# Optimization experiments

Measured on AMD Instinct MI355X. Metric: run time of the kernel, lower is better.

The kernel has to match this reference:

```python
import jax, jax.numpy as jnp
import numpy as np
import math

NUM_HEADS = 8

def setup_inputs() -> dict:
    key = jax.random.key(0)
    ks = jax.random.split(key, 5)
    b, h, w, c = 4, 128, 128, 256
    x = jax.random.normal(ks[0], (b, h, w, c), dtype=jnp.float32)
    scale = 1.0 / math.sqrt(c)  # keep weights reasonably scaled (kaiming-like)
    Wq = jax.random.normal(ks[1], (c, c), dtype=jnp.float32) * scale
    Wk = jax.random.normal(ks[2], (c, c), dtype=jnp.float32) * scale
    Wv = jax.random.normal(ks[3], (c, c), dtype=jnp.float32) * scale
    Wout = jax.random.normal(ks[4], (c, c), dtype=jnp.float32) * scale
    return {"x": x, "Wq": Wq, "Wk": Wk, "Wv": Wv, "Wout": Wout}

def reference(x, Wq, Wk, Wv, Wout):
    b, h, w, c = x.shape
    hw = h * w
    heads = NUM_HEADS
    dh = c // heads
    xs = x.reshape(b, hw, c)
    q = xs @ Wq  # (b, hw, c)
    k = xs @ Wk
    v = xs @ Wv

    def split_heads(t):
        # (b, hw, c) -> (b, c, hw) -> (b, heads, dh, hw)
        return t.transpose(0, 2, 1).reshape(b, heads, dh, hw)

    q = split_heads(q)
    k = split_heads(k)
    v = split_heads(v)
    # L2-normalize along the feature (hw) axis; original has no epsilon
    q = q / jnp.linalg.norm(q, axis=-1, keepdims=True)
    k = k / jnp.linalg.norm(k, axis=-1, keepdims=True)
    d_k = q.shape[-1]  # = hw
    attn = jnp.einsum('bhcd,bhed->bhce', q, k) / math.sqrt(d_k)  # (b,heads,dh,dh)
    attn = jax.nn.softmax(attn, axis=-1)
    vals = jnp.einsum('bhce,bhed->bhcd', attn, v)  # (b,heads,dh,hw)
    vals = vals.transpose(0, 3, 1, 2).reshape(b, hw, c)
    out = (vals @ Wout).reshape(b, h, w, c)
    return out
```

## Files before the change

### kernel.cpp

```cpp
#include <hip/hip_runtime.h>


#define B_   4
#define HW_  16384
#define C_   256

typedef __attribute__((ext_vector_type(8))) short short8;
typedef __attribute__((ext_vector_type(4))) float floatx4;

__device__ __forceinline__ unsigned short f2bf(float f) {
  unsigned u = __builtin_bit_cast(unsigned, f);
  u += 0x7FFFu + ((u >> 16) & 1u);
  return (unsigned short)(u >> 16);
}

__device__ __forceinline__ void gl_lds16(const unsigned short* g, unsigned short* l) {
  __builtin_amdgcn_global_load_lds(
      (const __attribute__((address_space(1))) unsigned int*)g,
      (__attribute__((address_space(3))) unsigned int*)l, 16, 0, 0);
}

__global__ __launch_bounds__(256) void k_cast_tr(const float* __restrict__ x,
                                                 unsigned short* __restrict__ xb,
                                                 unsigned short* __restrict__ xT) {
  __shared__ unsigned short lds[64][72];
  int bid = blockIdx.x;
  int t = threadIdx.x;
  int ct = bid & 3;
  int pt = (bid >> 2) & 255;
  int b  = bid >> 10;
  const float* src = x + ((size_t)(b * HW_ + pt * 64)) * C_ + ct * 64;
#pragma unroll
  for (int e = 0; e < 4; e++) {
    int lin = t + e * 256;
    int p = lin >> 4, c4 = lin & 15;
    float4 v = *(const float4*)(src + (size_t)p * C_ + c4 * 4);
    ushort4 h;
    h.x = f2bf(v.x); h.y = f2bf(v.y); h.z = f2bf(v.z); h.w = f2bf(v.w);
    *(ushort4*)(xb + ((size_t)(b * HW_ + pt * 64 + p)) * C_ + ct * 64 + c4 * 4) = h;
    lds[c4 * 4 + 0][p] = h.x;
    lds[c4 * 4 + 1][p] = h.y;
    lds[c4 * 4 + 2][p] = h.z;
    lds[c4 * 4 + 3][p] = h.w;
  }
  __syncthreads();
#pragma unroll
  for (int e = 0; e < 4; e++) {
    int lin = t + e * 256;
    int c = lin >> 4, p4 = lin & 15;
    ushort4 h;
    h.x = lds[c][p4 * 4 + 0];
    h.y = lds[c][p4 * 4 + 1];
    h.z = lds[c][p4 * 4 + 2];
    h.w = lds[c][p4 * 4 + 3];
    *(ushort4*)(xT + ((size_t)(b * C_ + ct * 64 + c)) * HW_ + pt * 64 + p4 * 4) = h;
  }
}

__global__ __launch_bounds__(256) void k_sgemm(const unsigned short* __restrict__ xT,
                                               float* __restrict__ part) {
  __shared__ unsigned short At[128 * 256];
  __shared__ unsigned short Bt[128 * 256];
  int bid = blockIdx.x;
  int ks = bid & 31, nt = (bid >> 5) & 1, mt = (bid >> 6) & 1, b = bid >> 7;
  const unsigned short* Ab = xT + ((size_t)(b * C_ + mt * 128)) * HW_ + ks * 512;
  const unsigned short* Bb = xT + ((size_t)(b * C_ + nt * 128)) * HW_ + ks * 512;
  int t = threadIdx.x, lane = t & 63, w = t >> 6;
  int wm = w >> 1, wn = w & 1;
  int l15 = lane & 15, l4 = lane >> 4;
  int lrow = lane >> 5;
  int lslot = lane & 31;
  floatx4 acc[4][4];
  floatx4 z = {0.f, 0.f, 0.f, 0.f};
#pragma unroll
  for (int i = 0; i < 4; i++)
#pragma unroll
    for (int j = 0; j < 4; j++) acc[i][j] = z;

  for (int ph = 0; ph < 2; ph++) {
    if (ph) __syncthreads();
#pragma unroll
    for (int i = 0; i < 16; i++) {
      int issue = w * 16 + i;
      int row = issue * 2 + lrow;
      int goct = lslot ^ (row & 31);
      gl_lds16(Ab + (size_t)row * HW_ + ph * 256 + goct * 8, At + issue * 512);
      gl_lds16(Bb + (size_t)row * HW_ + ph * 256 + goct * 8, Bt + issue * 512);
    }
    __syncthreads();
#pragma unroll
    for (int kk = 0; kk < 8; kk++) {
      short8 af[4], bfv[4];
      int oct = kk * 4 + l4;
#pragma unroll
      for (int tm = 0; tm < 4; tm++) {
        int row = wm * 64 + tm * 16 + l15;
        af[tm] = *(const short8*)(At + row * 256 + ((oct ^ (row & 31)) * 8));
      }
#pragma unroll
      for (int tn = 0; tn < 4; tn++) {
        int row = wn * 64 + tn * 16 + l15;
        bfv[tn] = *(const short8*)(Bt + row * 256 + ((oct ^ (row & 31)) * 8));
      }
#pragma unroll
      for (int tm = 0; tm < 4; tm++)
#pragma unroll
        for (int tn = 0; tn < 4; tn++)
          acc[tm][tn] = __builtin_amdgcn_mfma_f32_16x16x32_bf16(af[tm], bfv[tn],
                                                                acc[tm][tn], 0, 0, 0);
    }
  }
  float* pb = part + (size_t)bid * 16384;
#pragma unroll
  for (int tm = 0; tm < 4; tm++)
#pragma unroll
    for (int tn = 0; tn < 4; tn++)
#pragma unroll
      for (int r = 0; r < 4; r++) {
        int m = wm * 64 + tm * 16 + l4 * 4 + r;
        int n = wn * 64 + tn * 16 + l15;
        pb[m * 128 + n] = acc[tm][tn][r];
      }
}

__global__ __launch_bounds__(256) void k_sred(const float* __restrict__ part,
                                              float* __restrict__ S) {
  int idx = blockIdx.x * 256 + threadIdx.x;
  int b = idx >> 16;
  int m = (idx >> 8) & 255, n = idx & 255;
  const float* p = part + ((size_t)((b * 4 + (m >> 7) * 2 + (n >> 7)) * 32)) * 16384
                   + (m & 127) * 128 + (n & 127);
  float s = 0.f;
#pragma unroll
  for (int k = 0; k < 32; k++) s += p[k * 16384];
  S[idx] = s;
}

__global__ __launch_bounds__(256) void k_gemm_sw(const float* __restrict__ S,
                                                 const float* __restrict__ Wq,
                                                 const float* __restrict__ Wk,
                                                 float* __restrict__ SWq,
                                                 float* __restrict__ SWk) {
  __shared__ float As[64][17];
  __shared__ float Bs[16][65];
  int bid = blockIdx.x;
  int nt = bid & 7, mt = (bid >> 3) & 3, b = bid >> 5;
  int mb = mt * 64;
  const float* Wsel = (nt < 4) ? Wq : Wk;
  int nb = (nt & 3) * 64;
  int t = threadIdx.x, tx = t & 15, ty = t >> 4;
  float acc[4][4] = {};
  for (int kt = 0; kt < 16; kt++) {
    {
      int row = t >> 2, kq = t & 3;
      float4 v = *(const float4*)(S + ((size_t)(b * C_ + mb + row)) * C_ + kt * 16 + kq * 4);
      As[row][kq * 4 + 0] = v.x; As[row][kq * 4 + 1] = v.y;
      As[row][kq * 4 + 2] = v.z; As[row][kq * 4 + 3] = v.w;
    }
    {
      int kk = t >> 4, n4 = t & 15;
      float4 v = *(const float4*)(Wsel + ((size_t)(kt * 16 + kk)) * C_ + nb + n4 * 4);
      Bs[kk][n4 * 4 + 0] = v.x; Bs[kk][n4 * 4 + 1] = v.y;
      Bs[kk][n4 * 4 + 2] = v.z; Bs[kk][n4 * 4 + 3] = v.w;
    }
    __syncthreads();
#pragma unroll
    for (int k = 0; k < 16; k++) {
      float a[4], bb[4];
#pragma unroll
      for (int i = 0; i < 4; i++) a[i] = As[ty * 4 + i][k];
#pragma unroll
      for (int j = 0; j < 4; j++) bb[j] = Bs[k][tx * 4 + j];
#pragma unroll
      for (int i = 0; i < 4; i++)
#pragma unroll
        for (int j = 0; j < 4; j++) acc[i][j] += a[i] * bb[j];
    }
    __syncthreads();
  }
#pragma unroll
  for (int i = 0; i < 4; i++)
#pragma unroll
    for (int j = 0; j < 4; j++) {
      int row = mb + ty * 4 + i;
      int ng = nt * 64 + tx * 4 + j;
      if (ng < 256) SWq[((size_t)(b * C_ + row)) * C_ + ng] = acc[i][j];
      else          SWk[((size_t)(b * C_ + row)) * C_ + ng - 256] = acc[i][j];
    }
}

__global__ __launch_bounds__(256) void k_fuse(const float* __restrict__ Wq,
                                              const float* __restrict__ Wk,
                                              const float* __restrict__ SWq,
                                              const float* __restrict__ SWk,
                                              const float* __restrict__ Wout,
                                              float* __restrict__ U) {
  __shared__ float Wqh[256][32];
  __shared__ float Wkh[256][32];
  __shared__ float SWqh[256][32];
  __shared__ float SWkh[256][32];
  __shared__ float Lg[32][33];
  __shared__ float qp[8][32], kp[8][32], qin[32], kin[32];
  int b = blockIdx.x >> 3, h = blockIdx.x & 7;
  int t = threadIdx.x;
  int col = t & 31, rgrp = t >> 5;
  for (int r0 = 0; r0 < 256; r0 += 8) {
    int row = r0 + rgrp;
    Wqh[row][col]  = Wq[(size_t)row * C_ + h * 32 + col];
    Wkh[row][col]  = Wk[(size_t)row * C_ + h * 32 + col];
    SWqh[row][col] = SWq[((size_t)(b * C_ + row)) * C_ + h * 32 + col];
    SWkh[row][col] = SWk[((size_t)(b * C_ + row)) * C_ + h * 32 + col];
  }
  __syncthreads();
  {
    float g[4] = {0.f, 0.f, 0.f, 0.f};
    for (int k = 0; k < 256; k++) {
      float swk = SWkh[k][col];
#pragma unroll
      for (int r = 0; r < 4; r++) g[r] += Wqh[k][rgrp + 8 * r] * swk;
    }
#pragma unroll
    for (int r = 0; r < 4; r++) Lg[rgrp + 8 * r][col] = g[r];
  }
  {
    float sq = 0.f, sk = 0.f;
    for (int k = rgrp * 32; k < rgrp * 32 + 32; k++) {
      sq += Wqh[k][col] * SWqh[k][col];
      sk += Wkh[k][col] * SWkh[k][col];
    }
    qp[rgrp][col] = sq;
    kp[rgrp][col] = sk;
  }
  __syncthreads();
  if (t < 32) {
    float a = 0.f;
#pragma unroll
    for (int p = 0; p < 8; p++) a += qp[p][t];
    qin[t] = rsqrtf(a);
  } else if (t < 64) {
    int j = t - 32;
    float a = 0.f;
#pragma unroll
    for (int p = 0; p < 8; p++) a += kp[p][j];
    kin[j] = rsqrtf(a);
  }
  __syncthreads();
  if (t < 32) {
    float row[32];
    float mx = -1e30f;
#pragma unroll
    for (int j = 0; j < 32; j++) {
      row[j] = Lg[t][j] * qin[t] * kin[j] * 0.0078125f;
      mx = fmaxf(mx, row[j]);
    }
    float sum = 0.f;
#pragma unroll
    for (int j = 0; j < 32; j++) { row[j] = __expf(row[j] - mx); sum += row[j]; }
    float inv = 1.0f / sum;
#pragma unroll
    for (int j = 0; j < 32; j++) Lg[t][j] = row[j] * inv;
  }
  __syncthreads();
  float (*Wo)[256] = reinterpret_cast<float(*)[256]>(&Wqh[0][0]);
#pragma unroll
  for (int r = 0; r < 32; r++) Wo[r][t] = Wout[((size_t)(h * 32 + r)) * C_ + t];
  __syncthreads();
  for (int j = 0; j < 32; j++) {
    float a = 0.f;
#pragma unroll
    for (int i2 = 0; i2 < 32; i2++) a += Lg[i2][j] * Wo[i2][t];
    U[((size_t)(b * C_ + h * 32 + j)) * C_ + t] = a;
  }
}

__global__ __launch_bounds__(256) void k_gemm_w3(const float* __restrict__ Wv,
                                                 const float* __restrict__ U,
                                                 unsigned short* __restrict__ W3bT) {
  __shared__ float As[64][17];
  __shared__ float Bs[16][65];
  int bid = blockIdx.x;
  int nt = bid & 3, mt = (bid >> 2) & 3, b = bid >> 4;
  int mb = mt * 64, nb = nt * 64;
  int t = threadIdx.x, tx = t & 15, ty = t >> 4;
  float acc[4][4] = {};
  for (int kt = 0; kt < 16; kt++) {
    {
      int row = t >> 2, kq = t & 3;
      float4 v = *(const float4*)(Wv + ((size_t)(mb + row)) * C_ + kt * 16 + kq * 4);
      As[row][kq * 4 + 0] = v.x; As[row][kq * 4 + 1] = v.y;
      As[row][kq * 4 + 2] = v.z; As[row][kq * 4 + 3] = v.w;
    }
    {
      int kk = t >> 4, n4 = t & 15;
      float4 v = *(const float4*)(U + ((size_t)(b * C_ + kt * 16 + kk)) * C_ + nb + n4 * 4);
      Bs[kk][n4 * 4 + 0] = v.x; Bs[kk][n4 * 4 + 1] = v.y;
      Bs[kk][n4 * 4 + 2] = v.z; Bs[kk][n4 * 4 + 3] = v.w;
    }
    __syncthreads();
#pragma unroll
    for (int k = 0; k < 16; k++) {
      float a[4], bb[4];
#pragma unroll
      for (int i = 0; i < 4; i++) a[i] = As[ty * 4 + i][k];
#pragma unroll
      for (int j = 0; j < 4; j++) bb[j] = Bs[k][tx * 4 + j];
#pragma unroll
      for (int i = 0; i < 4; i++)
#pragma unroll
        for (int j = 0; j < 4; j++) acc[i][j] += a[i] * bb[j];
    }
    __syncthreads();
  }
#pragma unroll
  for (int i = 0; i < 4; i++)
#pragma unroll
    for (int j = 0; j < 4; j++)
      W3bT[((size_t)(b * C_ + nb + tx * 4 + j)) * C_ + mb + ty * 4 + i] = f2bf(acc[i][j]);
}

__global__ __launch_bounds__(256) void k_out(const unsigned short* __restrict__ xb,
                                             const unsigned short* __restrict__ W3bT,
                                             float* __restrict__ out) {
  __shared__ unsigned short At[128 * 64];
  __shared__ unsigned short Bt[128 * 64];
  int bid = blockIdx.x;
  int ntile = bid & 1, mtile = bid >> 1;
  int b = mtile >> 7;
  const unsigned short* Ab = xb + (size_t)mtile * 128 * C_;
  const unsigned short* Bb = W3bT + ((size_t)(b * C_ + ntile * 128)) * C_;
  int t = threadIdx.x, lane = t & 63, w = t >> 6;
  int wm = w >> 1, wn = w & 1;
  int l8 = lane >> 3, l7 = lane & 7;
  int srcoct = l7 ^ l8;
  int l15 = lane & 15, l4 = lane >> 4;
  floatx4 acc[4][4];
  floatx4 z = {0.f, 0.f, 0.f, 0.f};
#pragma unroll
  for (int i = 0; i < 4; i++)
#pragma unroll
    for (int j = 0; j < 4; j++) acc[i][j] = z;
  for (int s = 0; s < 4; s++) {
    if (s) __syncthreads();
#pragma unroll
    for (int i = 0; i < 4; i++) {
      int gi = w * 4 + i;
      int row = gi * 8 + l8;
      gl_lds16(Ab + (size_t)row * C_ + s * 64 + srcoct * 8, At + gi * 512);
      gl_lds16(Bb + (size_t)row * C_ + s * 64 + srcoct * 8, Bt + gi * 512);
    }
    __syncthreads();
#pragma unroll
    for (int kk = 0; kk < 2; kk++) {
      short8 af[4], bfv[4];
#pragma unroll
      for (int tm = 0; tm < 4; tm++) {
        int row = wm * 64 + tm * 16 + l15;
        int oct = kk * 4 + l4;
        af[tm] = *(const short8*)(At + row * 64 + ((oct ^ (l15 & 7)) * 8));
      }
#pragma unroll
      for (int tn = 0; tn < 4; tn++) {
        int row = wn * 64 + tn * 16 + l15;
        int oct = kk * 4 + l4;
        bfv[tn] = *(const short8*)(Bt + row * 64 + ((oct ^ (l15 & 7)) * 8));
      }
#pragma unroll
      for (int tm = 0; tm < 4; tm++)
#pragma unroll
        for (int tn = 0; tn < 4; tn++)
          acc[tm][tn] = __builtin_amdgcn_mfma_f32_16x16x32_bf16(af[tm], bfv[tn],
                                                                acc[tm][tn], 0, 0, 0);
    }
  }
  float* ob = out + (size_t)mtile * 128 * C_ + ntile * 128;
#pragma unroll
  for (int tm = 0; tm < 4; tm++)
#pragma unroll
    for (int tn = 0; tn < 4; tn++)
#pragma unroll
      for (int r = 0; r < 4; r++) {
        int m = wm * 64 + tm * 16 + l4 * 4 + r;
        int n = wn * 64 + tn * 16 + l15;
        ob[(size_t)m * C_ + n] = acc[tm][tn][r];
      }
}

extern "C" void kernel_launch(void* const* d_in, const int* in_sizes, int n_in,
                              void* d_out, int out_size, void* d_ws, size_t ws_size,
                              hipStream_t stream) {
  const float* x    = (const float*)d_in[0];
  const float* Wq   = (const float*)d_in[1];
  const float* Wk   = (const float*)d_in[2];
  const float* Wv   = (const float*)d_in[3];
  const float* Wout = (const float*)d_in[4];
  float* out = (float*)d_out;

  unsigned short* xT = (unsigned short*)d_ws;
  unsigned short* xb = xT + (size_t)16777216;
  float* part = (float*)(xb + (size_t)16777216);
  float* S    = part + (size_t)8388608;
  float* SWq  = S + 262144;
  float* SWk  = SWq + 262144;
  float* U    = SWk + 262144;
  unsigned short* W3bT = (unsigned short*)(U + 262144);

  k_cast_tr<<<dim3(4096), dim3(256), 0, stream>>>(x, xb, xT);
  k_sgemm<<<dim3(512), dim3(256), 0, stream>>>(xT, part);
  k_sred<<<dim3(1024), dim3(256), 0, stream>>>(part, S);
  k_gemm_sw<<<dim3(128), dim3(256), 0, stream>>>(S, Wq, Wk, SWq, SWk);
  k_fuse<<<dim3(32), dim3(256), 0, stream>>>(Wq, Wk, SWq, SWk, Wout, U);
  k_gemm_w3<<<dim3(64), dim3(256), 0, stream>>>(Wv, U, W3bT);
  k_out<<<dim3(1024), dim3(256), 0, stream>>>(xb, W3bT, out);
}
```

Baseline: 232.3 us.

## Drop bf16 x copy, fuse split-K reduction into SW gemm, halve splits

The cast kernel now writes only the transposed bf16 copy. The output GEMM reads fp32 x and fp32 W3T directly and converts to bf16 while staging into padded LDS, replacing the async global-to-LDS loads. The Gram GEMM uses 16 K-splits instead of 32, which halves the partial buffer. The separate reduction kernel is folded into the S·W GEMM, which also gets larger tiles. This removes one 32MB write and one kernel launch, but k_out now reads twice as many bytes of x, issues register-staged loads, and the fused SW kernel repeats the reduction for each block.

```diff
diff --git a/kernel.cpp b/kernel.cpp
--- a/kernel.cpp
+++ b/kernel.cpp
@@ -20,9 +20,8 @@
       (__attribute__((address_space(3))) unsigned int*)l, 16, 0, 0);
 }
 
-__global__ __launch_bounds__(256) void k_cast_tr(const float* __restrict__ x,
-                                                 unsigned short* __restrict__ xb,
-                                                 unsigned short* __restrict__ xT) {
+__global__ __launch_bounds__(256) void k_cast_t(const float* __restrict__ x,
+                                                unsigned short* __restrict__ xT) {
   __shared__ unsigned short lds[64][72];
   int bid = blockIdx.x;
   int t = threadIdx.x;
@@ -35,13 +34,10 @@
     int lin = t + e * 256;
     int p = lin >> 4, c4 = lin & 15;
     float4 v = *(const float4*)(src + (size_t)p * C_ + c4 * 4);
-    ushort4 h;
-    h.x = f2bf(v.x); h.y = f2bf(v.y); h.z = f2bf(v.z); h.w = f2bf(v.w);
-    *(ushort4*)(xb + ((size_t)(b * HW_ + pt * 64 + p)) * C_ + ct * 64 + c4 * 4) = h;
-    lds[c4 * 4 + 0][p] = h.x;
-    lds[c4 * 4 + 1][p] = h.y;
-    lds[c4 * 4 + 2][p] = h.z;
-    lds[c4 * 4 + 3][p] = h.w;
+    lds[c4 * 4 + 0][p] = f2bf(v.x);
+    lds[c4 * 4 + 1][p] = f2bf(v.y);
+    lds[c4 * 4 + 2][p] = f2bf(v.z);
+    lds[c4 * 4 + 3][p] = f2bf(v.w);
   }
   __syncthreads();
 #pragma unroll
@@ -62,9 +58,9 @@
   __shared__ unsigned short At[128 * 256];
   __shared__ unsigned short Bt[128 * 256];
   int bid = blockIdx.x;
-  int ks = bid & 31, nt = (bid >> 5) & 1, mt = (bid >> 6) & 1, b = bid >> 7;
-  const unsigned short* Ab = xT + ((size_t)(b * C_ + mt * 128)) * HW_ + ks * 512;
-  const unsigned short* Bb = xT + ((size_t)(b * C_ + nt * 128)) * HW_ + ks * 512;
+  int ks = bid & 15, nt = (bid >> 4) & 1, mt = (bid >> 5) & 1, b = bid >> 6;
+  const unsigned short* Ab = xT + ((size_t)(b * C_ + mt * 128)) * HW_ + ks * 1024;
+  const unsigned short* Bb = xT + ((size_t)(b * C_ + nt * 128)) * HW_ + ks * 1024;
   int t = threadIdx.x, lane = t & 63, w = t >> 6;
   int wm = w >> 1, wn = w & 1;
   int l15 = lane & 15, l4 = lane >> 4;
@@ -77,7 +73,7 @@
 #pragma unroll
     for (int j = 0; j < 4; j++) acc[i][j] = z;
 
-  for (int ph = 0; ph < 2; ph++) {
+  for (int ph = 0; ph < 4; ph++) {
     if (ph) __syncthreads();
 #pragma unroll
     for (int i = 0; i < 16; i++) {
@@ -123,70 +119,64 @@
       }
 }
 
-__global__ __launch_bounds__(256) void k_sred(const float* __restrict__ part,
-                                              float* __restrict__ S) {
-  int idx = blockIdx.x * 256 + threadIdx.x;
-  int b = idx >> 16;
-  int m = (idx >> 8) & 255, n = idx & 255;
-  const float* p = part + ((size_t)((b * 4 + (m >> 7) * 2 + (n >> 7)) * 32)) * 16384
-                   + (m & 127) * 128 + (n & 127);
-  float s = 0.f;
-#pragma unroll
-  for (int k = 0; k < 32; k++) s += p[k * 16384];
-  S[idx] = s;
-}
-
-__global__ __launch_bounds__(256) void k_gemm_sw(const float* __restrict__ S,
-                                                 const float* __restrict__ Wq,
-                                                 const float* __restrict__ Wk,
-                                                 float* __restrict__ SWq,
-                                                 float* __restrict__ SWk) {
-  __shared__ float As[64][17];
-  __shared__ float Bs[16][65];
+__global__ __launch_bounds__(256) void k_sw(const float* __restrict__ part,
+                                            const float* __restrict__ Wq,
+                                            const float* __restrict__ Wk,
+                                            float* __restrict__ SWq,
+                                            float* __restrict__ SWk) {
+  __shared__ float SsT[256][36];
+  __shared__ float Ws[128][132];
   int bid = blockIdx.x;
-  int nt = bid & 7, mt = (bid >> 3) & 3, b = bid >> 5;
-  int mb = mt * 64;
-  const float* Wsel = (nt < 4) ? Wq : Wk;
-  int nb = (nt & 3) * 64;
-  int t = threadIdx.x, tx = t & 15, ty = t >> 4;
+  int ns = bid & 3, ms = (bid >> 2) & 7, b = bid >> 5;
+  const float* Wsel = (ns < 2) ? Wq : Wk;
+  float* SWsel = (ns < 2) ? SWq : SWk;
+  int n0 = (ns & 1) * 128;
+  int t = threadIdx.x;
+  int nt_lane = t >> 7;
+  int cl = t & 127;
+#pragma unroll 4
+  for (int e = 0; e < 32; e++) {
+    int R = ms * 32 + e;
+    int mt = R >> 7;
+    const float* p = part + ((size_t)(((b * 2 + mt) * 2 + nt_lane) * 16)) * 16384
+                     + (R & 127) * 128 + cl;
+    float s = 0.f;
+#pragma unroll
+    for (int k = 0; k < 16; k++) s += p[(size_t)k * 16384];
+    SsT[t][e] = s;
+  }
+  int tx = t & 31, ty = t >> 5;
   float acc[4][4] = {};
-  for (int kt = 0; kt < 16; kt++) {
-    {
-      int row = t >> 2, kq = t & 3;
-      float4 v = *(const float4*)(S + ((size_t)(b * C_ + mb + row)) * C_ + kt * 16 + kq * 4);
-      As[row][kq * 4 + 0] = v.x; As[row][kq * 4 + 1] = v.y;
-      As[row][kq * 4 + 2] = v.z; As[row][kq * 4 + 3] = v.w;
-    }
-    {
-      int kk = t >> 4, n4 = t & 15;
-      float4 v = *(const float4*)(Wsel + ((size_t)(kt * 16 + kk)) * C_ + nb + n4 * 4);
-      Bs[kk][n4 * 4 + 0] = v.x; Bs[kk][n4 * 4 + 1] = v.y;
-      Bs[kk][n4 * 4 + 2] = v.z; Bs[kk][n4 * 4 + 3] = v.w;
+  for (int strip = 0; strip < 2; strip++) {
+    if (strip) __syncthreads();
+#pragma unroll
+    for (int e = 0; e < 16; e++) {
+      int idx = e * 256 + t;
+      int ml = idx >> 5, n4 = idx & 31;
+      float4 v = *(const float4*)(Wsel + ((size_t)(strip * 128 + ml)) * C_ + n0 + n4 * 4);
+      Ws[ml][n4 * 4 + 0] = v.x; Ws[ml][n4 * 4 + 1] = v.y;
+      Ws[ml][n4 * 4 + 2] = v.z; Ws[ml][n4 * 4 + 3] = v.w;
     }
     __syncthreads();
-#pragma unroll
-    for (int k = 0; k < 16; k++) {
-      float a[4], bb[4];
-#pragma unroll
-      for (int i = 0; i < 4; i++) a[i] = As[ty * 4 + i][k];
-#pragma unroll
-      for (int j = 0; j < 4; j++) bb[j] = Bs[k][tx * 4 + j];
+#pragma unroll 8
+    for (int ml = 0; ml < 128; ml++) {
+      int m = strip * 128 + ml;
+      float4 aq = *(const float4*)&SsT[m][ty * 4];
+      float4 bq = *(const float4*)&Ws[ml][tx * 4];
+      float av[4] = {aq.x, aq.y, aq.z, aq.w};
+      float bv[4] = {bq.x, bq.y, bq.z, bq.w};
 #pragma unroll
       for (int i = 0; i < 4; i++)
 #pragma unroll
-        for (int j = 0; j < 4; j++) acc[i][j] += a[i] * bb[j];
-    }
-    __syncthreads();
-  }
-#pragma unroll
-  for (int i = 0; i < 4; i++)
-#pragma unroll
-    for (int j = 0; j < 4; j++) {
-      int row = mb + ty * 4 + i;
-      int ng = nt * 64 + tx * 4 + j;
-      if (ng < 256) SWq[((size_t)(b * C_ + row)) * C_ + ng] = acc[i][j];
-      else          SWk[((size_t)(b * C_ + row)) * C_ + ng - 256] = acc[i][j];
-    }
+        for (int j = 0; j < 4; j++) acc[i][j] += av[i] * bv[j];
+    }
+  }
+#pragma unroll
+  for (int i = 0; i < 4; i++) {
+    int row = ms * 32 + ty * 4 + i;
+    float4 v = {acc[i][0], acc[i][1], acc[i][2], acc[i][3]};
+    *(float4*)(SWsel + ((size_t)(b * C_ + row)) * C_ + n0 + tx * 4) = v;
+  }
 }
 
 __global__ __launch_bounds__(256) void k_fuse(const float* __restrict__ Wq,
@@ -275,7 +265,7 @@
 
 __global__ __launch_bounds__(256) void k_gemm_w3(const float* __restrict__ Wv,
                                                  const float* __restrict__ U,
-                                                 unsigned short* __restrict__ W3bT) {
+                                                 float* __restrict__ W3T) {
   __shared__ float As[64][17];
   __shared__ float Bs[16][65];
   int bid = blockIdx.x;
@@ -315,23 +305,21 @@
   for (int i = 0; i < 4; i++)
 #pragma unroll
     for (int j = 0; j < 4; j++)
-      W3bT[((size_t)(b * C_ + nb + tx * 4 + j)) * C_ + mb + ty * 4 + i] = f2bf(acc[i][j]);
-}
-
-__global__ __launch_bounds__(256) void k_out(const unsigned short* __restrict__ xb,
-                                             const unsigned short* __restrict__ W3bT,
+      W3T[((size_t)(b * C_ + nb + tx * 4 + j)) * C_ + mb + ty * 4 + i] = acc[i][j];
+}
+
+__global__ __launch_bounds__(256) void k_out(const float* __restrict__ x,
+                                             const float* __restrict__ W3T,
                                              float* __restrict__ out) {
-  __shared__ unsigned short At[128 * 64];
-  __shared__ unsigned short Bt[128 * 64];
+  __shared__ unsigned short At[128 * 72];
+  __shared__ unsigned short Bt[128 * 72];
   int bid = blockIdx.x;
   int ntile = bid & 1, mtile = bid >> 1;
   int b = mtile >> 7;
-  const unsigned short* Ab = xb + (size_t)mtile * 128 * C_;
-  const unsigned short* Bb = W3bT + ((size_t)(b * C_ + ntile * 128)) * C_;
+  const float* Ab = x + (size_t)mtile * 128 * C_;
+  const float* Bb = W3T + ((size_t)(b * C_ + ntile * 128)) * C_;
   int t = threadIdx.x, lane = t & 63, w = t >> 6;
   int wm = w >> 1, wn = w & 1;
-  int l8 = lane >> 3, l7 = lane & 7;
-  int srcoct = l7 ^ l8;
   int l15 = lane & 15, l4 = lane >> 4;
   floatx4 acc[4][4];
   floatx4 z = {0.f, 0.f, 0.f, 0.f};
@@ -342,27 +330,31 @@
   for (int s = 0; s < 4; s++) {
     if (s) __syncthreads();
 #pragma unroll
-    for (int i = 0; i < 4; i++) {
-      int gi = w * 4 + i;
-      int row = gi * 8 + l8;
-      gl_lds16(Ab + (size_t)row * C_ + s * 64 + srcoct * 8, At + gi * 512);
-      gl_lds16(Bb + (size_t)row * C_ + s * 64 + srcoct * 8, Bt + gi * 512);
+    for (int e = 0; e < 8; e++) {
+      int idx = e * 256 + t;
+      int r = idx >> 4, c4 = idx & 15;
+      float4 va = *(const float4*)(Ab + (size_t)r * C_ + s * 64 + c4 * 4);
+      float4 vb = *(const float4*)(Bb + (size_t)r * C_ + s * 64 + c4 * 4);
+      ushort4 ha, hb;
+      ha.x = f2bf(va.x); ha.y = f2bf(va.y); ha.z = f2bf(va.z); ha.w = f2bf(va.w);
+      hb.x = f2bf(vb.x); hb.y = f2bf(vb.y); hb.z = f2bf(vb.z); hb.w = f2bf(vb.w);
+      *(ushort4*)(At + r * 72 + c4 * 4) = ha;
+      *(ushort4*)(Bt + r * 72 + c4 * 4) = hb;
     }
     __syncthreads();
 #pragma unroll
     for (int kk = 0; kk < 2; kk++) {
       short8 af[4], bfv[4];
+      int oct = kk * 4 + l4;
 #pragma unroll
       for (int tm = 0; tm < 4; tm++) {
         int row = wm * 64 + tm * 16 + l15;
-        int oct = kk * 4 + l4;
-        af[tm] = *(const short8*)(At + row * 64 + ((oct ^ (l15 & 7)) * 8));
+        af[tm] = *(const short8*)(At + row * 72 + oct * 8);
       }
 #pragma unroll
       for (int tn = 0; tn < 4; tn++) {
         int row = wn * 64 + tn * 16 + l15;
-        int oct = kk * 4 + l4;
-        bfv[tn] = *(const short8*)(Bt + row * 64 + ((oct ^ (l15 & 7)) * 8));
+        bfv[tn] = *(const short8*)(Bt + row * 72 + oct * 8);
       }
 #pragma unroll
       for (int tm = 0; tm < 4; tm++)
@@ -396,19 +388,16 @@
   float* out = (float*)d_out;
 
   unsigned short* xT = (unsigned short*)d_ws;
-  unsigned short* xb = xT + (size_t)16777216;
-  float* part = (float*)(xb + (size_t)16777216);
-  float* S    = part + (size_t)8388608;
-  float* SWq  = S + 262144;
+  float* part = (float*)(xT + (size_t)16777216);
+  float* SWq  = part + (size_t)4194304;
   float* SWk  = SWq + 262144;
   float* U    = SWk + 262144;
-  unsigned short* W3bT = (unsigned short*)(U + 262144);
-
-  k_cast_tr<<<dim3(4096), dim3(256), 0, stream>>>(x, xb, xT);
-  k_sgemm<<<dim3(512), dim3(256), 0, stream>>>(xT, part);
-  k_sred<<<dim3(1024), dim3(256), 0, stream>>>(part, S);
-  k_gemm_sw<<<dim3(128), dim3(256), 0, stream>>>(S, Wq, Wk, SWq, SWk);
+  float* W3T  = U + 262144;
+
+  k_cast_t<<<dim3(4096), dim3(256), 0, stream>>>(x, xT);
+  k_sgemm<<<dim3(256), dim3(256), 0, stream>>>(xT, part);
+  k_sw<<<dim3(128), dim3(256), 0, stream>>>(part, Wq, Wk, SWq, SWk);
   k_fuse<<<dim3(32), dim3(256), 0, stream>>>(Wq, Wk, SWq, SWk, Wout, U);
-  k_gemm_w3<<<dim3(64), dim3(256), 0, stream>>>(Wv, U, W3bT);
-  k_out<<<dim3(1024), dim3(256), 0, stream>>>(xb, W3bT, out);
-}
+  k_gemm_w3<<<dim3(64), dim3(256), 0, stream>>>(Wv, U, W3T);
+  k_out<<<dim3(1024), dim3(256), 0, stream>>>(x, W3T, out);
+}
```

Result: slower. 246.8 us (+6.2%).
